# Kernel tuning notes

Hardware: AMD Instinct MI355X
Metric: run time of the kernel (lower is better)

The kernel has to match this reference:

```python
import jax, jax.numpy as jnp
import numpy as np

EMBED = 1024
HEADS = 16
HEAD_DIM = EMBED // HEADS


def setup_inputs() -> dict:
    key = jax.random.key(0)
    ks = jax.random.split(key, 12)
    B, S = 2, 2048
    inp = {
        "query": jax.random.normal(ks[0], (B, S, EMBED), dtype=jnp.float32),
        "key": jax.random.normal(ks[1], (B, S, EMBED), dtype=jnp.float32),
        "value": jax.random.normal(ks[2], (B, S, EMBED), dtype=jnp.float32),
        "mask": jnp.ones((B, 1, 1, S), dtype=jnp.int32),
    }
    scale = 1.0 / np.sqrt(EMBED)
    inp["Wq"] = jax.random.normal(ks[3], (EMBED, EMBED), dtype=jnp.float32) * scale
    inp["bq"] = jax.random.normal(ks[4], (EMBED,), dtype=jnp.float32) * 0.01
    inp["Wk"] = jax.random.normal(ks[5], (EMBED, EMBED), dtype=jnp.float32) * scale
    inp["bk"] = jax.random.normal(ks[6], (EMBED,), dtype=jnp.float32) * 0.01
    inp["Wv"] = jax.random.normal(ks[7], (EMBED, EMBED), dtype=jnp.float32) * scale
    inp["bv"] = jax.random.normal(ks[8], (EMBED,), dtype=jnp.float32) * 0.01
    inp["Wo"] = jax.random.normal(ks[9], (EMBED, EMBED), dtype=jnp.float32) * scale
    inp["bo"] = jax.random.normal(ks[10], (EMBED,), dtype=jnp.float32) * 0.01
    return inp


def reference(query, key, value, mask, Wq, bq, Wk, bk, Wv, bv, Wo, bo):
    N, Lq, _ = query.shape
    Lk = key.shape[1]
    # Linear projections (torch Linear: x @ W.T + b)
    q = (query @ Wq.T + bq).reshape(N, Lq, HEADS, HEAD_DIM)
    k = (key @ Wk.T + bk).reshape(N, Lk, HEADS, HEAD_DIM)
    v = (value @ Wv.T + bv).reshape(N, Lk, HEADS, HEAD_DIM)
    # scores: [N, H, Lq, Lk]
    energy = jnp.einsum("nqhd,nkhd->nhqk", q, k)
    energy = jnp.where(mask == 0, jnp.float32(-1e20), energy)
    # NOTE: original scales by sqrt(embedSize), not sqrt(head_dim)
    attn = jax.nn.softmax(energy / jnp.sqrt(jnp.float32(EMBED)), axis=3)
    out = jnp.einsum("nhqv,nvhd->nqhd", attn, v).reshape(N, Lq, EMBED)
    return out @ Wo.T + bo
```

## Files before the change

### kernel.cpp

```cpp
#include <hip/hip_runtime.h>
#include <stdint.h>

typedef unsigned short u16;
typedef __attribute__((ext_vector_type(8))) short short8;
typedef __attribute__((ext_vector_type(4))) short short4v;
typedef __attribute__((ext_vector_type(4))) float floatx4;

#define AS_GLOBAL __attribute__((address_space(1)))
#define AS_LDS    __attribute__((address_space(3)))

#define QSCALE 0.045084220f

__device__ __forceinline__ float bf2f(u16 u) {
  union { unsigned int i; float f; } x; x.i = ((unsigned int)u) << 16; return x.f;
}
__device__ __forceinline__ u16 f2bf(float f) {
  union { float f; unsigned int i; } x; x.f = f;
  unsigned int u = x.i;
  u += 0x7fffu + ((u >> 16) & 1u);
  return (u16)(u >> 16);
}
__device__ __forceinline__ u16 f2bf_fast(float f) {
  union { float f; unsigned int i; } x; x.f = f;
  return (u16)((x.i + 0x8000u) >> 16);
}

__device__ __forceinline__ int probe_is_f32(const void* p) {
  const unsigned int* w = (const unsigned int*)p;
  int cnt = 0;
#pragma unroll
  for (int i = 0; i < 64; ++i) {
    unsigned int lo = w[i] & 0xFFFFu;
    int e = (int)((lo >> 7) & 0xFFu);
    cnt += (e >= 117 && e <= 137) ? 1 : 0;
  }
  return cnt < 32;
}

__device__ __forceinline__ short8 ld8(const void* P, size_t off, int isf32) {
  if (isf32) {
    const float* q = (const float*)P + off;
    float4 x = *(const float4*)q;
    float4 y = *(const float4*)(q + 4);
    short8 r;
    r[0] = (short)f2bf(x.x); r[1] = (short)f2bf(x.y);
    r[2] = (short)f2bf(x.z); r[3] = (short)f2bf(x.w);
    r[4] = (short)f2bf(y.x); r[5] = (short)f2bf(y.y);
    r[6] = (short)f2bf(y.z); r[7] = (short)f2bf(y.w);
    return r;
  }
  return *(const short8*)((const u16*)P + off);
}

__device__ __forceinline__ float ldscalar(const void* P, size_t idx, int isf32) {
  return isf32 ? ((const float*)P)[idx] : bf2f(((const u16*)P)[idx]);
}

__global__ __launch_bounds__(256) void cvt7(
    const void* s0, const void* s1, const void* s2, const void* s3,
    const void* s4, const void* s5, const void* s6,
    u16* d0, u16* d1, u16* d2, u16* d3, u16* d4, u16* d5, u16* d6)
{
  const int z = blockIdx.y;
  const void* src; u16* dst; int n;
  switch (z) {
    case 0: src = s0; dst = d0; n = 4194304; break;
    case 1: src = s1; dst = d1; n = 4194304; break;
    case 2: src = s2; dst = d2; n = 4194304; break;
    case 3: src = s3; dst = d3; n = 1048576; break;
    case 4: src = s4; dst = d4; n = 1048576; break;
    case 5: src = s5; dst = d5; n = 1048576; break;
    default: src = s6; dst = d6; n = 1048576; break;
  }
  const int isf32 = probe_is_f32(src);
  for (int i = blockIdx.x * 256 + threadIdx.x; i * 4 < n; i += gridDim.x * 256) {
    if (isf32) {
      float4 x = ((const float4*)src)[i];
      short4v r;
      r[0] = (short)f2bf(x.x); r[1] = (short)f2bf(x.y);
      r[2] = (short)f2bf(x.z); r[3] = (short)f2bf(x.w);
      *(short4v*)(dst + (size_t)i * 4) = r;
    } else {
      *(short4v*)(dst + (size_t)i * 4) = ((const short4v*)src)[i];
    }
  }
}

__device__ __forceinline__ void gemm_core_bf16(
    const u16* __restrict__ A, const u16* __restrict__ W,
    u16* As, u16* Bs, floatx4 acc[4][4], int m0, int n0, int K, int tid)
{
  const int lane = tid & 63, wv = tid >> 6;
  const int wm = wv >> 1, wn = wv & 1;
  const int g = lane >> 4, ml = lane & 15;
  const int r0 = tid >> 2, kc = (tid & 3) << 3;
  const u16* Ag0 = A + (size_t)(m0 + r0) * K + kc;
  const u16* Ag1 = A + (size_t)(m0 + r0 + 64) * K + kc;
  const u16* Bg0 = W + (size_t)(n0 + r0) * K + kc;
  const u16* Bg1 = W + (size_t)(n0 + r0 + 64) * K + kc;

#define STAGE_QKV(buf_, kt_) do {                                              \
    u16* a0 = As + (buf_) * 4096 + tid * 8;                                    \
    u16* b0 = Bs + (buf_) * 4096 + tid * 8;                                    \
    __builtin_amdgcn_global_load_lds((const AS_GLOBAL unsigned int*)(Ag0 + (kt_)), \
                                     (AS_LDS unsigned int*)a0, 16, 0, 0);      \
    __builtin_amdgcn_global_load_lds((const AS_GLOBAL unsigned int*)(Ag1 + (kt_)), \
                                     (AS_LDS unsigned int*)(a0 + 2048), 16, 0, 0); \
    __builtin_amdgcn_global_load_lds((const AS_GLOBAL unsigned int*)(Bg0 + (kt_)), \
                                     (AS_LDS unsigned int*)b0, 16, 0, 0);      \
    __builtin_amdgcn_global_load_lds((const AS_GLOBAL unsigned int*)(Bg1 + (kt_)), \
                                     (AS_LDS unsigned int*)(b0 + 2048), 16, 0, 0); \
  } while (0)

  STAGE_QKV(0, 0);
  int buf = 0;
#pragma unroll 2
  for (int kt = 0; kt < K; kt += 32) {
    const int nk = (kt + 32 < K) ? (kt + 32) : 0;
    STAGE_QKV(buf ^ 1, nk);
    __asm__ __volatile__("s_waitcnt vmcnt(4)\n\ts_barrier" ::: "memory");
    const u16* Ac = As + buf * 4096;
    const u16* Bc = Bs + buf * 4096;
    short8 af[4], bf[4];
#pragma unroll
    for (int i = 0; i < 4; ++i)
      af[i] = *(const short8*)(Ac + (wm * 64 + i * 16 + ml) * 32 + g * 8);
#pragma unroll
    for (int j = 0; j < 4; ++j)
      bf[j] = *(const short8*)(Bc + (wn * 64 + j * 16 + ml) * 32 + g * 8);
#pragma unroll
    for (int i = 0; i < 4; ++i)
#pragma unroll
      for (int j = 0; j < 4; ++j)
        acc[i][j] = __builtin_amdgcn_mfma_f32_16x16x32_bf16(af[i], bf[j], acc[i][j], 0, 0, 0);
    __asm__ __volatile__("s_waitcnt lgkmcnt(0)\n\ts_barrier" ::: "memory");
    buf ^= 1;
  }
#undef STAGE_QKV
  __asm__ __volatile__("s_waitcnt vmcnt(0)" ::: "memory");
}

__device__ __forceinline__ void gemm_core_cvt(
    const void* __restrict__ A, const void* __restrict__ W, int aF32, int bF32,
    u16* As, u16* Bs, floatx4 acc[4][4], int m0, int n0, int K, int tid)
{
  const int lane = tid & 63, wv = tid >> 6;
  const int wm = wv >> 1, wn = wv & 1;
  const int g = lane >> 4, ml = lane & 15;
  const int r0 = tid >> 2, kc = (tid & 3) << 3;
  const size_t offA0 = (size_t)(m0 + r0) * K + kc;
  const size_t offA1 = (size_t)(m0 + r0 + 64) * K + kc;
  const size_t offB0 = (size_t)(n0 + r0) * K + kc;
  const size_t offB1 = (size_t)(n0 + r0 + 64) * K + kc;
  u16* Al0 = As + tid * 8;  u16* Al1 = As + (tid + 256) * 8;
  u16* Bl0 = Bs + tid * 8;  u16* Bl1 = Bs + (tid + 256) * 8;
  for (int kt = 0; kt < K; kt += 32) {
    short8 a0 = ld8(A, offA0 + kt, aF32);
    short8 a1 = ld8(A, offA1 + kt, aF32);
    short8 b0 = ld8(W, offB0 + kt, bF32);
    short8 b1 = ld8(W, offB1 + kt, bF32);
    *(short8*)Al0 = a0;  *(short8*)Al1 = a1;
    *(short8*)Bl0 = b0;  *(short8*)Bl1 = b1;
    __syncthreads();
    short8 af[4], bf[4];
#pragma unroll
    for (int i = 0; i < 4; ++i)
      af[i] = *(const short8*)(As + (wm * 64 + i * 16 + ml) * 32 + g * 8);
#pragma unroll
    for (int j = 0; j < 4; ++j)
      bf[j] = *(const short8*)(Bs + (wn * 64 + j * 16 + ml) * 32 + g * 8);
#pragma unroll
    for (int i = 0; i < 4; ++i)
#pragma unroll
      for (int j = 0; j < 4; ++j)
        acc[i][j] = __builtin_amdgcn_mfma_f32_16x16x32_bf16(af[i], bf[j], acc[i][j], 0, 0, 0);
    __syncthreads();
  }
}

__device__ __forceinline__ void qkv_epilogue(
    floatx4 acc[4][4], const void* Bi, int cF32, u16* O, int m0, int n0,
    int tid, int z)
{
  const int lane = tid & 63, wv = tid >> 6;
  const int wm = wv >> 1, wn = wv & 1, g = lane >> 4, ml = lane & 15;
  const float sc = (z == 0) ? QSCALE : 1.0f;
#pragma unroll
  for (int j = 0; j < 4; ++j) {
    int gn = n0 + wn * 64 + j * 16 + ml;
    float bvv = ldscalar(Bi, (size_t)gn, cF32);
    int h = gn >> 6, d = gn & 63;
    if (z == 2) {
#pragma unroll
      for (int i = 0; i < 4; ++i) {
        int gm0 = m0 + wm * 64 + i * 16 + g * 4;
        int b = gm0 >> 11, s0 = gm0 & 2047;
        short4v pk;
#pragma unroll
        for (int r = 0; r < 4; ++r) pk[r] = (short)f2bf_fast(acc[i][j][r] + bvv);
        *(short4v*)(O + ((((size_t)b * 16 + h) * 64 + d) * 2048 + s0)) = pk;
      }
    } else {
#pragma unroll
      for (int i = 0; i < 4; ++i)
#pragma unroll
        for (int r = 0; r < 4; ++r) {
          int gm = m0 + wm * 64 + i * 16 + g * 4 + r;
          int b = gm >> 11, s = gm & 2047;
          O[(((size_t)b * 16 + h) * 2048 + s) * 64 + d] =
              f2bf_fast((acc[i][j][r] + bvv) * sc);
        }
    }
  }
}

__global__ __launch_bounds__(256) void qkv_gemm_bf16(
    const u16* __restrict__ Xq, const u16* __restrict__ Xk, const u16* __restrict__ Xv,
    const u16* __restrict__ Wq, const u16* __restrict__ Wk, const u16* __restrict__ Wv,
    const void* __restrict__ Bq, const void* __restrict__ Bk, const void* __restrict__ Bv,
    u16* __restrict__ Oq, u16* __restrict__ Ok, u16* __restrict__ Ov)
{
  __align__(16) __shared__ u16 As[8192];
  __align__(16) __shared__ u16 Bs[8192];
  const int z = blockIdx.z;
  const u16* X = (z == 0) ? Xq : (z == 1) ? Xk : Xv;
  const u16* W = (z == 0) ? Wq : (z == 1) ? Wk : Wv;
  const void* Bi = (z == 0) ? Bq : (z == 1) ? Bk : Bv;
  u16* O = (z == 0) ? Oq : (z == 1) ? Ok : Ov;
  const int tid = threadIdx.x;
  const int m0 = blockIdx.x * 128, n0 = blockIdx.y * 128;
  floatx4 acc[4][4] = {};
  gemm_core_bf16(X, W, As, Bs, acc, m0, n0, 1024, tid);
  const int cF32 = probe_is_f32(Bi);
  qkv_epilogue(acc, Bi, cF32, O, m0, n0, tid, z);
}

__global__ __launch_bounds__(256) void qkv_gemm_cvt(
    const void* __restrict__ Xq, const void* __restrict__ Xk, const void* __restrict__ Xv,
    const void* __restrict__ Wq, const void* __restrict__ Wk, const void* __restrict__ Wv,
    const void* __restrict__ Bq, const void* __restrict__ Bk, const void* __restrict__ Bv,
    u16* __restrict__ Oq, u16* __restrict__ Ok, u16* __restrict__ Ov)
{
  __align__(16) __shared__ u16 As[4096];
  __align__(16) __shared__ u16 Bs[4096];
  const int z = blockIdx.z;
  const void* X  = (z == 0) ? Xq : (z == 1) ? Xk : Xv;
  const void* W  = (z == 0) ? Wq : (z == 1) ? Wk : Wv;
  const void* Bi = (z == 0) ? Bq : (z == 1) ? Bk : Bv;
  u16* O = (z == 0) ? Oq : (z == 1) ? Ok : Ov;
  const int aF32 = probe_is_f32(X);
  const int bF32 = probe_is_f32(W);
  const int cF32 = probe_is_f32(Bi);
  const int tid = threadIdx.x;
  const int m0 = blockIdx.y * 128, n0 = blockIdx.x * 128;
  floatx4 acc[4][4] = {};
  gemm_core_cvt(X, W, aF32, bF32, As, Bs, acc, m0, n0, 1024, tid);
  qkv_epilogue(acc, Bi, cF32, O, m0, n0, tid, z);
}

__global__ __launch_bounds__(256) void out_gemm_bf16(
    const u16* __restrict__ X, const u16* __restrict__ W,
    const void* __restrict__ Bi, float* __restrict__ O)
{
  __align__(16) __shared__ u16 As[8192];
  __align__(16) __shared__ u16 Bs[8192];
  const int tid = threadIdx.x;
  const int m0 = blockIdx.x * 128, n0 = blockIdx.y * 128;
  floatx4 acc[4][4] = {};
  gemm_core_bf16(X, W, As, Bs, acc, m0, n0, 1024, tid);
  const int cF32 = probe_is_f32(Bi);
  const int lane = tid & 63, wv = tid >> 6;
  const int wm = wv >> 1, wn = wv & 1, g = lane >> 4, ml = lane & 15;
#pragma unroll
  for (int j = 0; j < 4; ++j) {
    int gn = n0 + wn * 64 + j * 16 + ml;
    float bvv = ldscalar(Bi, (size_t)gn, cF32);
#pragma unroll
    for (int i = 0; i < 4; ++i)
#pragma unroll
      for (int r = 0; r < 4; ++r) {
        int gm = m0 + wm * 64 + i * 16 + g * 4 + r;
        O[(size_t)gm * 1024 + gn] = acc[i][j][r] + bvv;
      }
  }
}

__global__ __launch_bounds__(256) void out_gemm_cvt(
    const u16* __restrict__ X, const void* __restrict__ W,
    const void* __restrict__ Bi, float* __restrict__ O)
{
  __align__(16) __shared__ u16 As[4096];
  __align__(16) __shared__ u16 Bs[4096];
  const int bF32 = probe_is_f32(W);
  const int cF32 = probe_is_f32(Bi);
  const int tid = threadIdx.x;
  const int m0 = blockIdx.y * 128, n0 = blockIdx.x * 128;
  floatx4 acc[4][4] = {};
  gemm_core_cvt(X, W, 0, bF32, As, Bs, acc, m0, n0, 1024, tid);
  const int lane = tid & 63, wv = tid >> 6;
  const int wm = wv >> 1, wn = wv & 1, g = lane >> 4, ml = lane & 15;
#pragma unroll
  for (int j = 0; j < 4; ++j) {
    int gn = n0 + wn * 64 + j * 16 + ml;
    float bvv = ldscalar(Bi, (size_t)gn, cF32);
#pragma unroll
    for (int i = 0; i < 4; ++i)
#pragma unroll
      for (int r = 0; r < 4; ++r) {
        int gm = m0 + wm * 64 + i * 16 + g * 4 + r;
        O[(size_t)gm * 1024 + gn] = acc[i][j][r] + bvv;
      }
  }
}

__global__ __launch_bounds__(256) void flash_attn(
    const u16* __restrict__ Q, const u16* __restrict__ K, const u16* __restrict__ V,
    const int* __restrict__ Mask, u16* __restrict__ O)
{
  __align__(16) __shared__ u16 Ks[64 * 64];
  __align__(16) __shared__ u16 Vt[64 * 64];
  __align__(16) __shared__ u16 Ps[4][16 * 72];
  __align__(16) __shared__ int Ms[64];
  __shared__ int Wok[4];

  const int qt = blockIdx.x;
  const int bh = blockIdx.y;
  const int b = bh >> 4, h = bh & 15;
  const int tid = threadIdx.x;
  const int lane = tid & 63, wv = tid >> 6;
  const int g = lane >> 4, ml = lane & 15;

  const size_t baseQ  = (((size_t)b * 16 + h) * 2048 + (size_t)qt * 64) * 64;
  const size_t baseKV = ((size_t)b * 16 + h) * 2048 * 64;

  {
    int la = 1;
#pragma unroll
    for (int i = 0; i < 8; ++i) la &= Mask[b * 2048 + tid * 8 + i];
    int wall = __all(la != 0);
    if (lane == 0) Wok[wv] = wall;
  }

  short8 qf[2];
#pragma unroll
  for (int ks = 0; ks < 2; ++ks)
    qf[ks] = *(const short8*)(Q + baseQ + (size_t)(wv * 16 + ml) * 64 + ks * 32 + g * 8);

  const u16* kg[2]; const u16* vg[2];
  u16* kl[2]; u16* vl[2];
#pragma unroll
  for (int t = 0; t < 2; ++t) {
    int s = tid + t * 256;
    int krow = s >> 3, kch = (s & 7) ^ (krow & 7);
    kg[t] = K + baseKV + (size_t)krow * 64 + kch * 8;
    int vd = s >> 3,  vch = (s & 7) ^ (vd & 7);
    vg[t] = V + baseKV + (size_t)vd * 2048 + vch * 8;
    kl[t] = Ks + (size_t)((tid & 448) + t * 256) * 8;
    vl[t] = Vt + (size_t)((tid & 448) + t * 256) * 8;
  }

  __syncthreads();
  const bool maskall = Wok[0] && Wok[1] && Wok[2] && Wok[3];

  floatx4 oacc[4] = {};
  float lp[4] = {0.f, 0.f, 0.f, 0.f};

  for (int kv0 = 0; kv0 < 2048; kv0 += 64) {
    __syncthreads();
#pragma unroll
    for (int t = 0; t < 2; ++t) {
      __builtin_amdgcn_global_load_lds((const AS_GLOBAL unsigned int*)kg[t],
                                       (AS_LDS unsigned int*)kl[t], 16, 0, 0);
      __builtin_amdgcn_global_load_lds((const AS_GLOBAL unsigned int*)vg[t],
                                       (AS_LDS unsigned int*)vl[t], 16, 0, 0);
      kg[t] += 64 * 64;
      vg[t] += 64;
    }
    if (!maskall && tid < 64) Ms[tid] = Mask[b * 2048 + kv0 + tid];
    __syncthreads();

    float sv[4][4];
#pragma unroll
    for (int j = 0; j < 4; ++j) {
      floatx4 a = {0.f, 0.f, 0.f, 0.f};
      int row = j * 16 + ml;
#pragma unroll
      for (int ks = 0; ks < 2; ++ks) {
        short8 kb = *(const short8*)(Ks + row * 64 + ((((ks << 2) + g) ^ (row & 7)) << 3));
        a = __builtin_amdgcn_mfma_f32_16x16x32_bf16(qf[ks], kb, a, 0, 0, 0);
      }
#pragma unroll
      for (int r = 0; r < 4; ++r) sv[j][r] = a[r];
    }
    if (!maskall) {
      int mok[4];
#pragma unroll
      for (int j = 0; j < 4; ++j) mok[j] = Ms[j * 16 + ml];
#pragma unroll
      for (int j = 0; j < 4; ++j)
#pragma unroll
        for (int r = 0; r < 4; ++r)
          sv[j][r] = (mok[j] == 0) ? -1.0e30f : sv[j][r];
    }

#pragma unroll
    for (int j = 0; j < 4; ++j)
#pragma unroll
      for (int r = 0; r < 4; ++r) {
        float p = __builtin_amdgcn_exp2f(sv[j][r]);
        sv[j][r] = p;
        lp[r] += p;
      }

#pragma unroll
    for (int j = 0; j < 4; ++j)
#pragma unroll
      for (int r = 0; r < 4; ++r)
        Ps[wv][(g * 4 + r) * 72 + j * 16 + ml] = f2bf_fast(sv[j][r]);

    __asm__ __volatile__("s_waitcnt lgkmcnt(0)" ::: "memory");

    short8 pa[2];
#pragma unroll
    for (int j2 = 0; j2 < 2; ++j2)
      pa[j2] = *(const short8*)(&Ps[wv][ml * 72 + j2 * 32 + g * 8]);
#pragma unroll
    for (int t = 0; t < 4; ++t)
#pragma unroll
      for (int j2 = 0; j2 < 2; ++j2) {
        short8 vb = *(const short8*)(Vt + (t * 16 + ml) * 64 + ((((j2 << 2) + g) ^ (ml & 7)) << 3));
        oacc[t] = __builtin_amdgcn_mfma_f32_16x16x32_bf16(pa[j2], vb, oacc[t], 0, 0, 0);
      }
  }

  float inv[4];
#pragma unroll
  for (int r = 0; r < 4; ++r) {
    float l = lp[r];
    l += __shfl_xor(l, 1);
    l += __shfl_xor(l, 2);
    l += __shfl_xor(l, 4);
    l += __shfl_xor(l, 8);
    inv[r] = (l > 0.f) ? 1.0f / l : 0.f;
  }
#pragma unroll
  for (int t = 0; t < 4; ++t)
#pragma unroll
    for (int r = 0; r < 4; ++r) {
      int q = qt * 64 + wv * 16 + g * 4 + r;
      int d = t * 16 + ml;
      O[((size_t)b * 2048 + q) * 1024 + h * 64 + d] = f2bf_fast(oacc[t][r] * inv[r]);
    }
}

extern "C" void kernel_launch(void* const* d_in, const int* in_sizes, int n_in,
                              void* d_out, int out_size, void* d_ws, size_t ws_size,
                              hipStream_t stream) {
  const void* q_in = d_in[0];
  const void* k_in = d_in[1];
  const void* v_in = d_in[2];
  const int* mask = (const int*)d_in[3];
  const void* Wq = d_in[4];  const void* bq = d_in[5];
  const void* Wk = d_in[6];  const void* bk = d_in[7];
  const void* Wv = d_in[8];  const void* bv = d_in[9];
  const void* Wo = d_in[10]; const void* bo = d_in[11];

  const size_t NTOK = (size_t)2 * 2048 * 1024;
  const size_t NW   = (size_t)1024 * 1024;

  if (ws_size >= (size_t)67108864) {
    u16* CXq = (u16*)d_ws;
    u16* CXk = CXq + NTOK;
    u16* CXv = CXk + NTOK;
    u16* CWq = CXv + NTOK;
    u16* CWk = CWq + NW;
    u16* CWv = CWk + NW;
    u16* CWo = CWv + NW;
    u16* Qp  = CWo + NW;
    u16* Kp  = Qp + NTOK;
    u16* Vp  = Kp + NTOK;
    u16* Ao  = Vp + NTOK;

    cvt7<<<dim3(1024, 7), 256, 0, stream>>>(q_in, k_in, v_in, Wq, Wk, Wv, Wo,
                                            CXq, CXk, CXv, CWq, CWk, CWv, CWo);
    qkv_gemm_bf16<<<dim3(32, 8, 3), 256, 0, stream>>>(CXq, CXk, CXv,
                                                      CWq, CWk, CWv,
                                                      bq, bk, bv, Qp, Kp, Vp);
    flash_attn<<<dim3(32, 32), 256, 0, stream>>>(Qp, Kp, Vp, mask, Ao);
    out_gemm_bf16<<<dim3(32, 8), 256, 0, stream>>>(Ao, CWo, bo, (float*)d_out);
  } else {
    u16* Qp = (u16*)d_ws;
    u16* Kp = Qp + NTOK;
    u16* Vp = Kp + NTOK;
    u16* Ao = Vp + NTOK;

    qkv_gemm_cvt<<<dim3(8, 32, 3), 256, 0, stream>>>(q_in, k_in, v_in,
                                                     Wq, Wk, Wv, bq, bk, bv,
                                                     Qp, Kp, Vp);
    flash_attn<<<dim3(32, 32), 256, 0, stream>>>(Qp, Kp, Vp, mask, Ao);
    out_gemm_cvt<<<dim3(8, 32), 256, 0, stream>>>(Ao, Wo, bo, (float*)d_out);
  }
}
```

Baseline: 257.9 us.

## Double-buffer K tiles and overlap V load with QK compute in flash attention

K tiles now go into a double-buffered LDS array, and the next K tile is prefetched while the current one is used. The V tile load is issued at the start of each iteration and waited on only after the softmax, just before the PV matmul. Explicit vmcnt waits and s_barrier replace the __syncthreads pairs, and s_setprio is raised around the MFMA sections. The aim is to hide global-to-LDS latency behind compute, at the cost of more LDS and fragile hand-counted vmcnt values. The mask load Mask[...] is a regular global load that also counts in vmcnt, which may make those counts off when the mask is not all ones.

Measured after the change: 266.0 us. 3.1% more time.

```diff
diff --git a/kernel.cpp b/kernel.cpp
--- a/kernel.cpp
+++ b/kernel.cpp
@@ -317,7 +317,7 @@
     const u16* __restrict__ Q, const u16* __restrict__ K, const u16* __restrict__ V,
     const int* __restrict__ Mask, u16* __restrict__ O)
 {
-  __align__(16) __shared__ u16 Ks[64 * 64];
+  __align__(16) __shared__ u16 Ks[2][64 * 64];
   __align__(16) __shared__ u16 Vt[64 * 64];
   __align__(16) __shared__ u16 Ps[4][16 * 72];
   __align__(16) __shared__ int Ms[64];
@@ -347,7 +347,7 @@
     qf[ks] = *(const short8*)(Q + baseQ + (size_t)(wv * 16 + ml) * 64 + ks * 32 + g * 8);
 
   const u16* kg[2]; const u16* vg[2];
-  u16* kl[2]; u16* vl[2];
+  int lo[2];
 #pragma unroll
   for (int t = 0; t < 2; ++t) {
     int s = tid + t * 256;
@@ -355,9 +355,13 @@
     kg[t] = K + baseKV + (size_t)krow * 64 + kch * 8;
     int vd = s >> 3,  vch = (s & 7) ^ (vd & 7);
     vg[t] = V + baseKV + (size_t)vd * 2048 + vch * 8;
-    kl[t] = Ks + (size_t)((tid & 448) + t * 256) * 8;
-    vl[t] = Vt + (size_t)((tid & 448) + t * 256) * 8;
-  }
+    lo[t] = ((tid & 448) + t * 256) * 8;
+  }
+
+#pragma unroll
+  for (int t = 0; t < 2; ++t)
+    __builtin_amdgcn_global_load_lds((const AS_GLOBAL unsigned int*)kg[t],
+                                     (AS_LDS unsigned int*)(&Ks[0][0] + lo[t]), 16, 0, 0);
 
   __syncthreads();
   const bool maskall = Wok[0] && Wok[1] && Wok[2] && Wok[3];
@@ -365,33 +369,37 @@
   floatx4 oacc[4] = {};
   float lp[4] = {0.f, 0.f, 0.f, 0.f};
 
+  int buf = 0;
+#pragma unroll 2
   for (int kv0 = 0; kv0 < 2048; kv0 += 64) {
-    __syncthreads();
-#pragma unroll
-    for (int t = 0; t < 2; ++t) {
-      __builtin_amdgcn_global_load_lds((const AS_GLOBAL unsigned int*)kg[t],
-                                       (AS_LDS unsigned int*)kl[t], 16, 0, 0);
-      __builtin_amdgcn_global_load_lds((const AS_GLOBAL unsigned int*)vg[t],
-                                       (AS_LDS unsigned int*)vl[t], 16, 0, 0);
-      kg[t] += 64 * 64;
-      vg[t] += 64;
-    }
+#pragma unroll
+    for (int t = 0; t < 2; ++t)
+      __builtin_amdgcn_global_load_lds((const AS_GLOBAL unsigned int*)(vg[t] + kv0),
+                                       (AS_LDS unsigned int*)(Vt + lo[t]), 16, 0, 0);
+    const int nxt = (kv0 + 64) & 2047;
+#pragma unroll
+    for (int t = 0; t < 2; ++t)
+      __builtin_amdgcn_global_load_lds((const AS_GLOBAL unsigned int*)(kg[t] + (size_t)nxt * 64),
+                                       (AS_LDS unsigned int*)(&Ks[buf ^ 1][0] + lo[t]), 16, 0, 0);
     if (!maskall && tid < 64) Ms[tid] = Mask[b * 2048 + kv0 + tid];
-    __syncthreads();
-
+    __asm__ __volatile__("s_waitcnt vmcnt(4) lgkmcnt(0)\n\ts_barrier" ::: "memory");
+
+    const u16* Kc = &Ks[buf][0];
     float sv[4][4];
+    __builtin_amdgcn_s_setprio(1);
 #pragma unroll
     for (int j = 0; j < 4; ++j) {
       floatx4 a = {0.f, 0.f, 0.f, 0.f};
       int row = j * 16 + ml;
 #pragma unroll
       for (int ks = 0; ks < 2; ++ks) {
-        short8 kb = *(const short8*)(Ks + row * 64 + ((((ks << 2) + g) ^ (row & 7)) << 3));
+        short8 kb = *(const short8*)(Kc + row * 64 + ((((ks << 2) + g) ^ (row & 7)) << 3));
         a = __builtin_amdgcn_mfma_f32_16x16x32_bf16(qf[ks], kb, a, 0, 0, 0);
       }
 #pragma unroll
       for (int r = 0; r < 4; ++r) sv[j][r] = a[r];
     }
+    __builtin_amdgcn_s_setprio(0);
     if (!maskall) {
       int mok[4];
 #pragma unroll
@@ -418,12 +426,14 @@
       for (int r = 0; r < 4; ++r)
         Ps[wv][(g * 4 + r) * 72 + j * 16 + ml] = f2bf_fast(sv[j][r]);
 
+    __asm__ __volatile__("s_waitcnt vmcnt(2)\n\ts_barrier" ::: "memory");
     __asm__ __volatile__("s_waitcnt lgkmcnt(0)" ::: "memory");
 
     short8 pa[2];
 #pragma unroll
     for (int j2 = 0; j2 < 2; ++j2)
       pa[j2] = *(const short8*)(&Ps[wv][ml * 72 + j2 * 32 + g * 8]);
+    __builtin_amdgcn_s_setprio(1);
 #pragma unroll
     for (int t = 0; t < 4; ++t)
 #pragma unroll
@@ -431,7 +441,12 @@
         short8 vb = *(const short8*)(Vt + (t * 16 + ml) * 64 + ((((j2 << 2) + g) ^ (ml & 7)) << 3));
         oacc[t] = __builtin_amdgcn_mfma_f32_16x16x32_bf16(pa[j2], vb, oacc[t], 0, 0, 0);
       }
-  }
+    __builtin_amdgcn_s_setprio(0);
+
+    __asm__ __volatile__("s_barrier" ::: "memory");
+    buf ^= 1;
+  }
+  __asm__ __volatile__("s_waitcnt vmcnt(0)" ::: "memory");
 
   float inv[4];
 #pragma unroll
```
